# Kernel tuning notes

Measured on AMD Instinct MI355X. Metric: run time of the kernel, lower is better.

Reference implementation:

```python
import jax, jax.numpy as jnp
import numpy as np

ALPHA = 1.0
NEG = -1e20  # matches torch code's -1e+20 padding for impossible cells


def setup_inputs() -> dict:
    key = jax.random.key(0)
    W = jax.random.normal(key, (32, 512, 1024), dtype=jnp.float32)
    return {"W": W}


def _combine(x, y):
    # associative operator for the log-space linear recurrence
    # m_j = logaddexp(m_{j-1} + a_j, b_j)
    a1, b1 = x
    a2, b2 = y
    return (a1 + a2, jnp.logaddexp(b1 + a2, b2))


def _forward(W):
    # Faithful to BayesianDTW.compute_location / compute_location_new:
    #   mu[:,0,:] = mu[:,:,0] = -1e20, mu[:,0,0] = 0
    #   mu[i,j] = logsumexp(mu[i-1,j], mu[i,j-1], mu[i-1,j-1]) + alpha*W[i-1,j-1]
    # Implemented as a row scan; the within-row left-neighbor dependency is a
    # log-space linear recurrence solved with an associative scan (O(Na*log Nb)
    # depth instead of O(Na*Nb) sequential steps).
    B, Na, Nb = W.shape
    aW = ALPHA * W  # [B, Na, Nb]
    row0 = jnp.concatenate(
        [jnp.zeros((B, 1), W.dtype), jnp.full((B, Nb), NEG, W.dtype)], axis=1
    )  # mu[:, 0, :]

    def step(prev_row, w_row):
        # prev_row: mu[:, i-1, :] -> [B, Nb+1]; w_row: alpha*W[:, i-1, :] -> [B, Nb]
        c = jnp.logaddexp(prev_row[:, 1:], prev_row[:, :-1])  # top + top-left
        # mu[i,j] = logaddexp(mu[i,j-1] + w_j, c_j + w_j), mu[i,0] = NEG
        A, Bc = jax.lax.associative_scan(_combine, (w_row, c + w_row), axis=1)
        m = jnp.logaddexp(NEG + A, Bc)  # include mu[i,0] = NEG initial carry
        new_row = jnp.concatenate(
            [jnp.full((m.shape[0], 1), NEG, m.dtype), m], axis=1
        )
        return new_row, new_row

    _, rows = jax.lax.scan(step, row0, jnp.transpose(aW, (1, 0, 2)))  # [Na, B, Nb+1]
    mu = jnp.concatenate([row0[:, None, :], jnp.transpose(rows, (1, 0, 2))], axis=1)
    return mu  # [B, Na+1, Nb+1], scale=False behavior


def reference(W):
    return _forward(W)
```

## Files before the change

kernel.cpp:

```cpp
#include <hip/hip_runtime.h>
#include <stdint.h>
#include <stddef.h>


#define NBATCH  32
#define NA      512
#define NB      1024
#define NSTRIPE 8
#define SW      128
#define CH      16
#define NCHUNK  (NA / CH)
#define LSTR    128
#define OROWS   513
#define OCOLS   1025
#define FSTRIDE 32

#define NEGV    (-1e20f)
#define LOG2E   (1.4426950408889634f)
#define LN2     (0.6931471805599453f)
#define NEG2    (-1.4426950408889634e20f)
#define FLAGTAG 0x5A000000u

#define EXP2F(x) __builtin_amdgcn_exp2f(x)
#define LOG2F(x) __builtin_amdgcn_logf(x)

__device__ __forceinline__ void gl_lds(const float* g, float* l) {
    __builtin_amdgcn_global_load_lds(
        (const __attribute__((address_space(1))) void*)g,
        (__attribute__((address_space(3))) void*)l, 4, 0, 0);
}

__device__ __forceinline__ float lse3_2(float a, float b, float c) {
    float m = fmaxf(fmaxf(a, b), c);
    float s = EXP2F(a - m) + EXP2F(b - m) + EXP2F(c - m);
    return m + LOG2F(s);
}

__device__ __forceinline__ float rdlane(float v, int l) {
    return __int_as_float(__builtin_amdgcn_readlane(__float_as_int(v), l));
}

__device__ __forceinline__ float lane_shr1(float x, int lane) {
    int xi  = __float_as_int(x);
    int shr = __builtin_amdgcn_update_dpp(0, xi, 0x111, 0xf, 0xf, true);
    float v = __int_as_float(shr);
    float a15 = rdlane(x, 15), a31 = rdlane(x, 31), a47 = rdlane(x, 47);
    v = (lane == 16) ? a15 : v;
    v = (lane == 32) ? a31 : v;
    v = (lane == 48) ? a47 : v;
    return v;
}

__device__ __forceinline__ unsigned int ld_flag(unsigned int* fp) {
    return __hip_atomic_load(fp, __ATOMIC_RELAXED, __HIP_MEMORY_SCOPE_AGENT);
}
__device__ __forceinline__ void st_flag(unsigned int* fp, unsigned int v) {
    __hip_atomic_store(fp, v, __ATOMIC_RELAXED, __HIP_MEMORY_SCOPE_AGENT);
}
__device__ __forceinline__ float ld_edge(const float* p) {
    return __hip_atomic_load((float*)p, __ATOMIC_RELAXED, __HIP_MEMORY_SCOPE_AGENT);
}
__device__ __forceinline__ void st_edge(float* p, float v) {
    __hip_atomic_store(p, v, __ATOMIC_RELAXED, __HIP_MEMORY_SCOPE_AGENT);
}

__device__ __forceinline__ void wait_flag(unsigned int* fp, unsigned int need) {
    for (int k = 0; k < (1 << 22); ++k) {
        unsigned int v = ld_flag(fp);
        if ((v >> 24) == 0x5Au && (v & 0x00FFFFFFu) >= need) break;
    }
    asm volatile("" ::: "memory");
}

__global__ __launch_bounds__(64, 1)
void dtw_pipe(const float* __restrict__ W, float* __restrict__ out,
              unsigned int* __restrict__ flags)
{
    __shared__ float lds_w[128 * LSTR];
    __shared__ float lds_o[128 * LSTR];

    const int lane = (int)threadIdx.x;
    const int bid  = (int)blockIdx.x;
    const int b    = bid & (NBATCH - 1);
    const int s    = bid >> 5;

    const float*  Wb  = W + ((size_t)b * NA) * NB + s * SW;
    float*        ob  = out + (size_t)b * OROWS * OCOLS;
    unsigned int* fmy = flags + (size_t)bid * FSTRIDE;
    unsigned int* fup = flags + (size_t)(bid - NBATCH) * FSTRIDE;

    ob[s * SW + 1 + lane]      = NEGV;
    ob[s * SW + 1 + 64 + lane] = NEGV;
    if (s == 0) {
        if (lane == 0) ob[0] = 0.0f;
        for (int r = lane; r < NA; r += 64)
            ob[(size_t)(r + 1) * OCOLS] = NEGV;
    }

    for (int q = 0; q < 3; ++q) {
        const float* wsrc = Wb + (size_t)q * CH * NB;
        for (int rr = 0; rr < CH; ++rr) {
            const int slot = q * CH + rr;
            gl_lds(wsrc + (size_t)rr * NB + lane,      &lds_w[slot * LSTR]);
            gl_lds(wsrc + (size_t)rr * NB + 64 + lane, &lds_w[slot * LSTR + 64]);
        }
    }

    float evcur = -1e30f, evnxt = -1e30f, lres = -1e30f;
    if (s > 0) {
        wait_flag(fup, 1u);
        if (lane < CH)
            evcur = ld_edge(&ob[(size_t)(1 + lane) * OCOLS + s * SW]) * LOG2E;
        wait_flag(fup, 2u);
        if (lane < CH)
            evnxt = ld_edge(&ob[(size_t)(CH + 1 + lane) * OCOLS + s * SW]) * LOG2E;
        wait_flag(fup, 3u);
        if (lane < CH)
            lres  = ld_edge(&ob[(size_t)(2 * CH + 1 + lane) * OCOLS + s * SW]) * LOG2E;
    }

    asm volatile("s_waitcnt vmcnt(0)" ::: "memory");

    float topA = NEG2, topB = NEG2;
    float sh_in = NEG2;
    float tl_reg = NEG2;
    float ev_im1 = (s == 0) ? 0.0f : NEG2;
    unsigned int fpoll = 0;

    float2 w_cur = *(const float2*)&lds_w[((0 - lane) & 127) * LSTR + 2 * lane];
    float2 w_nx1 = *(const float2*)&lds_w[((1 - lane) & 127) * LSTR + 2 * lane];

    auto step = [&](int m_, int tt) {
        const int t = (m_ << 4) + tt;
        const int r = t - lane;
        if (tt == 1 && s > 0) fpoll = ld_flag(fup);
        float2 w_pre = *(const float2*)&lds_w[((r + 2) & 127) * LSTR + 2 * lane];
        const float ev_i = rdlane(evcur, tt);
        const float lf = (lane == 0) ? ev_i   : sh_in;
        const float tl = (lane == 0) ? ev_im1 : tl_reg;
        const float uA = fmaf(w_cur.x, LOG2E, lse3_2(topA, lf, tl));
        const float uB = fmaf(w_cur.y, LOG2E, lse3_2(topB, uA, topA));
        const bool on = (r >= 0);
        if (on & (r < NA)) {
            *(float2*)&lds_o[(r & 127) * LSTR + 2 * lane]
                = make_float2(uA * LN2, uB * LN2);
        }
        topA   = on ? uA : NEG2;
        topB   = on ? uB : NEG2;
        tl_reg = on ? lf : NEG2;
        ev_im1 = ev_i;
        sh_in  = lane_shr1(uB, lane);
        w_cur = w_nx1; w_nx1 = w_pre;
    };

    for (int m = 0; m < 35; ++m) {
        #pragma unroll
        for (int tt = 0; tt < 16; ++tt) step(m, tt);

        const int f = m - 4;
        if (s < NSTRIPE - 1 && f >= 0 && lane < CH) {
            const int rw = (f << 4) + lane;
            const float evl = lds_o[(rw & 127) * LSTR + 127];
            st_edge(ob + (size_t)(rw + 1) * OCOLS + (s + 1) * SW, evl);
        }
        asm volatile("s_waitcnt vmcnt(1)" ::: "memory");
        if (s < NSTRIPE - 1 && f >= 1 && lane == 0)
            st_flag(fmy, FLAGTAG + (unsigned)f);
        if (f >= 0) {
            #pragma unroll
            for (int rr = 0; rr < CH; ++rr) {
                const int rw = (f << 4) + rr;
                const float v0 = lds_o[(rw & 127) * LSTR + lane];
                const float v1 = lds_o[(rw & 127) * LSTR + 64 + lane];
                float* orow = ob + (size_t)(rw + 1) * OCOLS + s * SW + 1;
                orow[lane]      = v0;
                orow[64 + lane] = v1;
            }
        }
        evcur = evnxt; evnxt = lres;
        const int c = m + 3;
        if (s > 0 && c < NCHUNK) {
            const unsigned need = (unsigned)(m + 4);
            if (!((fpoll >> 24) == 0x5Au && (fpoll & 0x00FFFFFFu) >= need))
                wait_flag(fup, need);
            lres = -1e30f;
            if (lane < CH)
                lres = ld_edge(&ob[(size_t)((c << 4) + 1 + lane) * OCOLS + s * SW])
                       * LOG2E;
        }
        if (c < NCHUNK) {
            const float* wsrc = Wb + (size_t)(c << 4) * NB;
            #pragma unroll
            for (int rr = 0; rr < CH; ++rr) {
                const int slot = ((c << 4) + rr) & 127;
                gl_lds(wsrc + (size_t)rr * NB + lane,      &lds_w[slot * LSTR]);
                gl_lds(wsrc + (size_t)rr * NB + 64 + lane, &lds_w[slot * LSTR + 64]);
            }
        }
    }

    #pragma unroll
    for (int tt = 0; tt < 15; ++tt) step(35, tt);

    {
        const int f = NCHUNK - 1;
        if (s < NSTRIPE - 1 && lane < CH) {
            const int rw = (f << 4) + lane;
            const float evl = lds_o[(rw & 127) * LSTR + 127];
            st_edge(ob + (size_t)(rw + 1) * OCOLS + (s + 1) * SW, evl);
        }
        asm volatile("s_waitcnt vmcnt(1)" ::: "memory");
        if (s < NSTRIPE - 1 && lane == 0)
            st_flag(fmy, FLAGTAG + (unsigned)(NCHUNK - 1));
        #pragma unroll
        for (int rr = 0; rr < CH; ++rr) {
            const int rw = (f << 4) + rr;
            const float v0 = lds_o[(rw & 127) * LSTR + lane];
            const float v1 = lds_o[(rw & 127) * LSTR + 64 + lane];
            float* orow = ob + (size_t)(rw + 1) * OCOLS + s * SW + 1;
            orow[lane]      = v0;
            orow[64 + lane] = v1;
        }
        asm volatile("s_waitcnt vmcnt(0)" ::: "memory");
        if (s < NSTRIPE - 1 && lane == 0)
            st_flag(fmy, FLAGTAG + (unsigned)NCHUNK);
    }
}

extern "C" void kernel_launch(void* const* d_in, const int* in_sizes, int n_in,
                              void* d_out, int out_size, void* d_ws, size_t ws_size,
                              hipStream_t stream) {
    const float*  W     = (const float*)d_in[0];
    float*        out   = (float*)d_out;
    unsigned int* flags = (unsigned int*)d_ws;
    (void)in_sizes; (void)n_in; (void)out_size; (void)ws_size;
    hipLaunchKernelGGL(dtw_pipe, dim3(NBATCH * NSTRIPE), dim3(64), 0, stream,
                       W, out, flags);
}
```

Before: 419.0 us.

## Halve sync chunk size, stream W into registers, and specialize wavefront phases

Reduces the per-stripe chunk from 16 to 8 rows, so downstream stripes get their edge flags sooner and the cross-stripe pipeline fills faster. The LDS staging buffer for W and its global_load_lds prefetch are replaced by a 4-deep rotating register prefetch that loads each lane's float2 straight from global memory every step. The log-sum-exp of three values now uses max/med3/min, which drops one exp2. The main loop is split into startup, steady and drain phases so the steady phase skips the r>=0 and r<NA predication. This adds a global load with short prefetch distance on every step and more frequent flag traffic, so memory latency may now sit on the critical path.

```diff
diff --git a/kernel.cpp b/kernel.cpp
--- a/kernel.cpp
+++ b/kernel.cpp
@@ -8,7 +8,7 @@
 #define NB      1024
 #define NSTRIPE 8
 #define SW      128
-#define CH      16
+#define CH      8
 #define NCHUNK  (NA / CH)
 #define LSTR    128
 #define OROWS   513
@@ -24,16 +24,12 @@
 #define EXP2F(x) __builtin_amdgcn_exp2f(x)
 #define LOG2F(x) __builtin_amdgcn_logf(x)
 
-__device__ __forceinline__ void gl_lds(const float* g, float* l) {
-    __builtin_amdgcn_global_load_lds(
-        (const __attribute__((address_space(1))) void*)g,
-        (__attribute__((address_space(3))) void*)l, 4, 0, 0);
-}
-
 __device__ __forceinline__ float lse3_2(float a, float b, float c) {
-    float m = fmaxf(fmaxf(a, b), c);
-    float s = EXP2F(a - m) + EXP2F(b - m) + EXP2F(c - m);
-    return m + LOG2F(s);
+    float m  = fmaxf(fmaxf(a, b), c);
+    float md = __builtin_amdgcn_fmed3f(a, b, c);
+    float mn = fminf(fminf(a, b), c);
+    float ss = 1.0f + EXP2F(md - m) + EXP2F(mn - m);
+    return m + LOG2F(ss);
 }
 
 __device__ __forceinline__ float rdlane(float v, int l) {
@@ -76,7 +72,6 @@
 void dtw_pipe(const float* __restrict__ W, float* __restrict__ out,
               unsigned int* __restrict__ flags)
 {
-    __shared__ float lds_w[128 * LSTR];
     __shared__ float lds_o[128 * LSTR];
 
     const int lane = (int)threadIdx.x;
@@ -97,13 +92,12 @@
             ob[(size_t)(r + 1) * OCOLS] = NEGV;
     }
 
-    for (int q = 0; q < 3; ++q) {
-        const float* wsrc = Wb + (size_t)q * CH * NB;
-        for (int rr = 0; rr < CH; ++rr) {
-            const int slot = q * CH + rr;
-            gl_lds(wsrc + (size_t)rr * NB + lane,      &lds_w[slot * LSTR]);
-            gl_lds(wsrc + (size_t)rr * NB + 64 + lane, &lds_w[slot * LSTR + 64]);
-        }
+    float2 wr[4];
+    #pragma unroll
+    for (int k = 0; k < 4; ++k) {
+        int rowc = k - lane;
+        rowc = rowc < 0 ? 0 : rowc;
+        wr[k] = *(const float2*)&Wb[(size_t)rowc * NB + 2 * lane];
     }
 
     float evcur = -1e30f, evnxt = -1e30f, lres = -1e30f;
@@ -127,49 +121,54 @@
     float ev_im1 = (s == 0) ? 0.0f : NEG2;
     unsigned int fpoll = 0;
 
-    float2 w_cur = *(const float2*)&lds_w[((0 - lane) & 127) * LSTR + 2 * lane];
-    float2 w_nx1 = *(const float2*)&lds_w[((1 - lane) & 127) * LSTR + 2 * lane];
-
-    auto step = [&](int m_, int tt) {
-        const int t = (m_ << 4) + tt;
+    auto stepc = [&](int m, int tt, bool GATE, bool GNA) {
+        const int t = 8 * m + tt;
         const int r = t - lane;
         if (tt == 1 && s > 0) fpoll = ld_flag(fup);
-        float2 w_pre = *(const float2*)&lds_w[((r + 2) & 127) * LSTR + 2 * lane];
+        const float2 wv = wr[tt & 3];
+        {
+            int rowc = r + 4;
+            rowc = rowc < 0 ? 0 : (rowc > NA - 1 ? NA - 1 : rowc);
+            wr[tt & 3] = *(const float2*)&Wb[(size_t)rowc * NB + 2 * lane];
+        }
         const float ev_i = rdlane(evcur, tt);
         const float lf = (lane == 0) ? ev_i   : sh_in;
         const float tl = (lane == 0) ? ev_im1 : tl_reg;
-        const float uA = fmaf(w_cur.x, LOG2E, lse3_2(topA, lf, tl));
-        const float uB = fmaf(w_cur.y, LOG2E, lse3_2(topB, uA, topA));
-        const bool on = (r >= 0);
-        if (on & (r < NA)) {
+        const float uA = fmaf(wv.x, LOG2E, lse3_2(topA, lf, tl));
+        const float uB = fmaf(wv.y, LOG2E, lse3_2(topB, uA, topA));
+        bool db = true;
+        if (GATE) db = (r >= 0);
+        if (GNA)  db = (r < NA);
+        if (db) {
             *(float2*)&lds_o[(r & 127) * LSTR + 2 * lane]
                 = make_float2(uA * LN2, uB * LN2);
         }
-        topA   = on ? uA : NEG2;
-        topB   = on ? uB : NEG2;
-        tl_reg = on ? lf : NEG2;
+        if (GATE) {
+            const bool on = (r >= 0);
+            topA   = on ? uA : NEG2;
+            topB   = on ? uB : NEG2;
+            tl_reg = on ? lf : NEG2;
+        } else {
+            topA = uA; topB = uB; tl_reg = lf;
+        }
         ev_im1 = ev_i;
         sh_in  = lane_shr1(uB, lane);
-        w_cur = w_nx1; w_nx1 = w_pre;
     };
 
-    for (int m = 0; m < 35; ++m) {
-        #pragma unroll
-        for (int tt = 0; tt < 16; ++tt) step(m, tt);
-
-        const int f = m - 4;
+    auto boundary = [&](int m) {
+        const int f = m - 8;
         if (s < NSTRIPE - 1 && f >= 0 && lane < CH) {
-            const int rw = (f << 4) + lane;
+            const int rw = (f << 3) + lane;
             const float evl = lds_o[(rw & 127) * LSTR + 127];
             st_edge(ob + (size_t)(rw + 1) * OCOLS + (s + 1) * SW, evl);
         }
-        asm volatile("s_waitcnt vmcnt(1)" ::: "memory");
+        asm volatile("s_waitcnt vmcnt(4)" ::: "memory");
         if (s < NSTRIPE - 1 && f >= 1 && lane == 0)
             st_flag(fmy, FLAGTAG + (unsigned)f);
         if (f >= 0) {
             #pragma unroll
             for (int rr = 0; rr < CH; ++rr) {
-                const int rw = (f << 4) + rr;
+                const int rw = (f << 3) + rr;
                 const float v0 = lds_o[(rw & 127) * LSTR + lane];
                 const float v1 = lds_o[(rw & 127) * LSTR + 64 + lane];
                 float* orow = ob + (size_t)(rw + 1) * OCOLS + s * SW + 1;
@@ -185,36 +184,42 @@
                 wait_flag(fup, need);
             lres = -1e30f;
             if (lane < CH)
-                lres = ld_edge(&ob[(size_t)((c << 4) + 1 + lane) * OCOLS + s * SW])
+                lres = ld_edge(&ob[(size_t)((c << 3) + 1 + lane) * OCOLS + s * SW])
                        * LOG2E;
         }
-        if (c < NCHUNK) {
-            const float* wsrc = Wb + (size_t)(c << 4) * NB;
-            #pragma unroll
-            for (int rr = 0; rr < CH; ++rr) {
-                const int slot = ((c << 4) + rr) & 127;
-                gl_lds(wsrc + (size_t)rr * NB + lane,      &lds_w[slot * LSTR]);
-                gl_lds(wsrc + (size_t)rr * NB + 64 + lane, &lds_w[slot * LSTR + 64]);
-            }
-        }
-    }
-
+    };
+
+    for (int m = 0; m < 8; ++m) {
+        #pragma unroll
+        for (int tt = 0; tt < 8; ++tt) stepc(m, tt, true, false);
+        boundary(m);
+    }
+    for (int m = 8; m < 64; ++m) {
+        #pragma unroll
+        for (int tt = 0; tt < 8; ++tt) stepc(m, tt, false, false);
+        boundary(m);
+    }
+    for (int m = 64; m < 71; ++m) {
+        #pragma unroll
+        for (int tt = 0; tt < 8; ++tt) stepc(m, tt, false, true);
+        boundary(m);
+    }
     #pragma unroll
-    for (int tt = 0; tt < 15; ++tt) step(35, tt);
+    for (int tt = 0; tt < 7; ++tt) stepc(71, tt, false, true);
 
     {
         const int f = NCHUNK - 1;
         if (s < NSTRIPE - 1 && lane < CH) {
-            const int rw = (f << 4) + lane;
+            const int rw = (f << 3) + lane;
             const float evl = lds_o[(rw & 127) * LSTR + 127];
             st_edge(ob + (size_t)(rw + 1) * OCOLS + (s + 1) * SW, evl);
         }
         asm volatile("s_waitcnt vmcnt(1)" ::: "memory");
         if (s < NSTRIPE - 1 && lane == 0)
-            st_flag(fmy, FLAGTAG + (unsigned)(NCHUNK - 1));
+            st_flag(fmy, FLAGTAG + (unsigned)f);
         #pragma unroll
         for (int rr = 0; rr < CH; ++rr) {
-            const int rw = (f << 4) + rr;
+            const int rw = (f << 3) + rr;
             const float v0 = lds_o[(rw & 127) * LSTR + lane];
             const float v1 = lds_o[(rw & 127) * LSTR + 64 + lane];
             float* orow = ob + (size_t)(rw + 1) * OCOLS + s * SW + 1;
```

New measurement: 417.7 us. No clear change (-0.3%).
